# Optimization experiments

Measured on AMD Instinct MI355X. Metric: run time of the kernel, lower is better.

The kernel has to match this reference:

```python
import jax, jax.numpy as jnp
import numpy as np

ALPHA = 0.01        # NoiseLayer gaussian scale
P_FEAT = 0.5        # feature dropout (NoiseLayer and TransForm_W)
P_EDGE = 0.4        # graph_corr edge-value dropout
BN_EPS = 1e-5


def setup_inputs() -> dict:
    key = jax.random.key(0)
    k1, k2, k3, k4 = jax.random.split(key, 4)
    N, E, D_IN, D_H = 100000, 1600000, 512, 128
    data = jax.random.normal(k1, (N, D_IN), dtype=jnp.float32)
    adj_indices = jax.random.randint(k2, (2, E), 0, N, dtype=jnp.int64)
    adj_values = jax.random.uniform(k3, (E,), dtype=jnp.float32)
    W = jax.random.normal(k4, (D_IN, D_H), dtype=jnp.float32) * (6.0 / (D_IN + D_H)) ** 0.5
    gamma = jnp.ones((D_H,), dtype=jnp.float32)
    beta = jnp.zeros((D_H,), dtype=jnp.float32)
    return {"data": data, "adj_indices": adj_indices, "adj_values": adj_values,
            "W": W, "gamma": gamma, "beta": beta}


def reference(data, adj_indices, adj_values, W, gamma, beta):
    N = data.shape[0]
    kn, kd1, kd2, ke = jax.random.split(jax.random.key(42), 4)

    # NoiseLayer: x + alpha*randn, then dropout(p=0.5)
    x = data + ALPHA * jax.random.normal(kn, data.shape, data.dtype)
    keep = 1.0 - P_FEAT
    x = x * jax.random.bernoulli(kd1, keep, x.shape).astype(x.dtype) / keep

    # TransForm_W: dropout(p=0.5) then x @ W  -> [N, hidden]
    x = x * jax.random.bernoulli(kd2, keep, x.shape).astype(x.dtype) / keep
    h = x @ W

    # edge-value dropout (graph_corr=0.4) + sparse spmm via segment_sum
    keep_e = 1.0 - P_EDGE
    vals = adj_values * jax.random.bernoulli(ke, keep_e, adj_values.shape).astype(adj_values.dtype) / keep_e
    row, col = adj_indices[0], adj_indices[1]
    msg = vals[:, None] * h[col]                       # [E, hidden]
    agg = jax.ops.segment_sum(msg, row, num_segments=N)  # [N, hidden]

    # ELU activation
    feat = jax.nn.elu(agg)

    # BatchNorm1d (training mode, batch stats over nodes), view_type='spatial'
    mean = feat.mean(axis=0)
    var = feat.var(axis=0)
    feat = gamma * (feat - mean) * jax.lax.rsqrt(var + BN_EPS) + beta
    return feat
```

## Files before the change

kernel.cpp:

```cpp
#include <hip/hip_runtime.h>
#include <stdint.h>

#define N_NODES 100000
#define D_IN 512
#define D_H 128
#define N_EDGES 1600000

__host__ __device__ __forceinline__ void threefry2x32(uint32_t k0, uint32_t k1,
                                                      uint32_t x0, uint32_t x1,
                                                      uint32_t& o0, uint32_t& o1) {
  uint32_t k2 = k0 ^ k1 ^ 0x1BD11BDAu;
  x0 += k0; x1 += k1;
#if defined(__HIP_DEVICE_COMPILE__)
#define ROTL(v, r) __builtin_rotateleft32((v), (r))
#else
#define ROTL(v, r) (((v) << (r)) | ((v) >> (32 - (r))))
#endif
#define TFR(r) x0 += x1; x1 = ROTL(x1, r); x1 ^= x0;
  TFR(13) TFR(15) TFR(26) TFR(6)
  x0 += k1; x1 += k2 + 1u;
  TFR(17) TFR(29) TFR(16) TFR(24)
  x0 += k2; x1 += k0 + 2u;
  TFR(13) TFR(15) TFR(26) TFR(6)
  x0 += k0; x1 += k1 + 3u;
  TFR(17) TFR(29) TFR(16) TFR(24)
  x0 += k1; x1 += k2 + 4u;
  TFR(13) TFR(15) TFR(26) TFR(6)
  x0 += k2; x1 += k0 + 5u;
#undef TFR
#undef ROTL
  o0 = x0; o1 = x1;
}

__device__ __forceinline__ uint32_t tf_bits(uint32_t k0, uint32_t k1, uint32_t i) {
  uint32_t w0, w1;
  threefry2x32(k0, k1, 0u, i, w0, w1);
  return w0 ^ w1;
}

__device__ __forceinline__ float bits_to_unit(uint32_t b) {
  return __uint_as_float((b >> 9) | 0x3f800000u) - 1.0f;
}

__device__ __forceinline__ unsigned short f2bf(float f) {
  uint32_t b = __float_as_uint(f);
  return (unsigned short)((b + 0x7FFFu + ((b >> 16) & 1u)) >> 16);
}

__device__ __forceinline__ float erfinv_fast(float x) {
  float w = -__logf(fmaf(-x, x, 1.0f));
  float wc = w - 2.5f;
  float p = 2.81022636e-08f;
  p = fmaf(p, wc, 3.43273939e-07f);
  p = fmaf(p, wc, -3.5233877e-06f);
  p = fmaf(p, wc, -4.39150654e-06f);
  p = fmaf(p, wc, 0.00021858087f);
  p = fmaf(p, wc, -0.00125372503f);
  p = fmaf(p, wc, -0.00417768164f);
  p = fmaf(p, wc, 0.246640727f);
  p = fmaf(p, wc, 1.50140941f);
  float wt = fmaf(w, rsqrtf(w), -3.0f);
  float q = -0.000200214257f;
  q = fmaf(q, wt, 0.000100950558f);
  q = fmaf(q, wt, 0.00134934322f);
  q = fmaf(q, wt, -0.00367342844f);
  q = fmaf(q, wt, 0.00573950773f);
  q = fmaf(q, wt, -0.0076224613f);
  q = fmaf(q, wt, 0.00943887047f);
  q = fmaf(q, wt, 1.00167406f);
  q = fmaf(q, wt, 2.83297682f);
  return ((w < 5.0f) ? p : q) * x;
}

#define PE 0.60000002384185791f
#define GS_BLKS 2048

__global__ __launch_bounds__(256) void prep_kernel(
    const int* __restrict__ adj32, int* __restrict__ flag,
    int* __restrict__ counts, float* __restrict__ stats,
    const float* __restrict__ W, unsigned short* __restrict__ Wt) {
  int idx = blockIdx.x * 256 + threadIdx.x;
  if (blockIdx.x == 0 && threadIdx.x < 64) {
    bool hi_zero = (adj32[2 * threadIdx.x + 1] == 0);
    unsigned long long bl = __ballot(hi_zero);
    if (threadIdx.x == 0) *flag = (bl == ~0ull) ? 1 : 0;
  }
  if (idx < N_NODES) counts[idx] = 0;
  if (idx < 256) stats[idx] = 0.0f;
  if (idx < D_IN * D_H) {
    int k = idx >> 7, n = idx & 127;
    Wt[n * 512 + k] = f2bf(W[idx]);
  }
}

#define MAIN_CHUNKS 31250

__global__ __launch_bounds__(256) void fused_kernel(
    const float* __restrict__ data, unsigned short* __restrict__ x,
    const int* __restrict__ adj32, const int* __restrict__ flag,
    int* __restrict__ counts,
    uint32_t kn0, uint32_t kn1, uint32_t kd10, uint32_t kd11,
    uint32_t kd20, uint32_t kd21, uint32_t ke0, uint32_t ke1) {
  __shared__ uint2 queue[4][512];
  __shared__ unsigned short res[4][512];
  const int wave = threadIdx.x >> 6, lane = threadIdx.x & 63;
  for (uint32_t c = blockIdx.x; c < MAIN_CHUNKS; c += gridDim.x) {
    if ((c % 5u) == 4u) {
      uint32_t e = (c / 5u) * 256u + threadIdx.x;
      int fl = *flag;
      int r = fl ? adj32[2 * e] : adj32[e];
      uint32_t eb = tf_bits(ke0, ke1, e);
      if (bits_to_unit(eb) < PE) atomicAdd(&counts[r], 1);
      continue;
    }
    uint32_t gblk = (c / 5u) * 4u + (c % 5u);
    const uint32_t wbase = gblk * 2048u + (uint32_t)wave * 512u;
    const uint32_t i0 = wbase + (uint32_t)lane * 8u;
    float4 d0 = *(const float4*)(data + i0);
    float4 d1 = *(const float4*)(data + i0 + 4);
    float dv[8] = {d0.x, d0.y, d0.z, d0.w, d1.x, d1.y, d1.z, d1.w};
    *(uint4*)(&res[wave][lane * 8]) = make_uint4(0u, 0u, 0u, 0u);

    uint32_t qc = 0;
#pragma unroll
    for (int j = 0; j < 8; ++j) {
      uint32_t ab = tf_bits(kd10, kd11, i0 + (uint32_t)j);
      bool keep = (ab >> 31) == 0u;
      unsigned long long m = __ballot(keep);
      uint32_t below = __builtin_amdgcn_mbcnt_hi(
          (uint32_t)(m >> 32), __builtin_amdgcn_mbcnt_lo((uint32_t)m, 0u));
      if (keep)
        queue[wave][qc + below] =
            make_uint2(__float_as_uint(dv[j]), (uint32_t)(lane * 8 + j));
      qc += (uint32_t)__popcll(m);
    }

    uint32_t qc2 = 0;
    for (uint32_t k0 = 0; k0 < qc; k0 += 64) {
      uint32_t k = k0 + (uint32_t)lane;
      bool act = k < qc;
      uint2 ent = make_uint2(0u, 0u);
      if (act) ent = queue[wave][k];
      uint32_t bb = tf_bits(kd20, kd21, wbase + ent.y);
      bool keep = act && ((bb >> 31) == 0u);
      unsigned long long m = __ballot(keep);
      uint32_t below = __builtin_amdgcn_mbcnt_hi(
          (uint32_t)(m >> 32), __builtin_amdgcn_mbcnt_lo((uint32_t)m, 0u));
      if (keep) queue[wave][qc2 + below] = ent;
      qc2 += (uint32_t)__popcll(m);
    }

    for (uint32_t k0 = 0; k0 < qc2; k0 += 64) {
      uint32_t k = k0 + (uint32_t)lane;
      bool act = k < qc2;
      uint2 ent = make_uint2(0u, 0u);
      if (act) ent = queue[wave][k];
      uint32_t nb = tf_bits(kn0, kn1, wbase + ent.y);
      float f = bits_to_unit(nb);
      float u = fmaf(f, 2.0f, -0.99999994f);
      float z = erfinv_fast(u);
      float val = fmaf(0.0141421356237f, z, __uint_as_float(ent.x));
      unsigned short r = f2bf(val * 4.0f);
      if (act) res[wave][ent.y] = r;
    }

    uint4 rr = *(const uint4*)(&res[wave][lane * 8]);
    *(uint4*)(x + i0) = rr;
  }
}

typedef __attribute__((ext_vector_type(8))) short bf16x8;
typedef __attribute__((ext_vector_type(4))) float f32x4;
typedef _Float16 half8 __attribute__((ext_vector_type(8)));
#define BM 64
#define BK 64
#define LDT 72

__global__ __launch_bounds__(256) void gemm_kernel(
    const unsigned short* __restrict__ x, const unsigned short* __restrict__ Wt,
    unsigned short* __restrict__ hh) {
  __shared__ __align__(16) unsigned short a_lds[BM * LDT];
  __shared__ __align__(16) unsigned short b_lds[128 * LDT];
  const int tid = threadIdx.x;
  const int r0 = blockIdx.x * BM;
  const int wave = tid >> 6, lane = tid & 63;
  const int lane15 = lane & 15, quad = lane >> 4;
  const int waveM = (wave & 1) * 32, waveN = (wave >> 1) * 64;
  f32x4 acc[2][4] = {};
  for (int kc = 0; kc < D_IN; kc += BK) {
    __syncthreads();
    {
      int row = tid >> 2, q = tid & 3;
      int gr = r0 + row;
      uint4 v0 = make_uint4(0, 0, 0, 0), v1 = v0;
      if (gr < N_NODES) {
        const unsigned short* src = x + (size_t)gr * D_IN + kc + q * 16;
        v0 = *(const uint4*)(src);
        v1 = *(const uint4*)(src + 8);
      }
      *(uint4*)(a_lds + row * LDT + q * 16) = v0;
      *(uint4*)(a_lds + row * LDT + q * 16 + 8) = v1;
    }
    {
      int n = tid >> 1, half = tid & 1;
      const uint4* src = (const uint4*)(Wt + n * 512 + kc + half * 32);
      uint4* dst = (uint4*)(b_lds + n * LDT + half * 32);
      dst[0] = src[0]; dst[1] = src[1]; dst[2] = src[2]; dst[3] = src[3];
    }
    __syncthreads();
    for (int ks = 0; ks < BK; ks += 32) {
      bf16x8 afrag[2], bfrag[4];
      for (int m = 0; m < 2; ++m)
        afrag[m] = *(const bf16x8*)(a_lds + (waveM + m * 16 + lane15) * LDT + ks + quad * 8);
      for (int n = 0; n < 4; ++n)
        bfrag[n] = *(const bf16x8*)(b_lds + (waveN + n * 16 + lane15) * LDT + ks + quad * 8);
      for (int m = 0; m < 2; ++m)
        for (int n = 0; n < 4; ++n)
          acc[m][n] = __builtin_amdgcn_mfma_f32_16x16x32_bf16(afrag[m], bfrag[n], acc[m][n], 0, 0, 0);
    }
  }
  for (int m = 0; m < 2; ++m) {
    int growb = r0 + waveM + m * 16 + quad * 4;
    for (int r = 0; r < 4; ++r) {
      int grow = growb + r;
      if (grow < N_NODES)
        for (int n = 0; n < 4; ++n) {
          _Float16 hv = (_Float16)acc[m][n][r];
          hh[(size_t)grow * D_H + waveN + n * 16 + lane15] =
              __builtin_bit_cast(unsigned short, hv);
        }
    }
  }
}

#define SCAN_B 512
#define SCAN_NBLK ((N_NODES + SCAN_B - 1) / SCAN_B)

__global__ __launch_bounds__(256) void scan1_kernel(const int* __restrict__ counts,
                                                    int* __restrict__ rowstart,
                                                    int* __restrict__ bsums) {
  __shared__ int bufA[SCAN_B], bufB[SCAN_B];
  int t = threadIdx.x, b = blockIdx.x;
  int g0 = b * SCAN_B + t, g1 = g0 + 256;
  int v0 = (g0 < N_NODES) ? counts[g0] : 0;
  int v1 = (g1 < N_NODES) ? counts[g1] : 0;
  bufA[t] = v0; bufA[t + 256] = v1;
  __syncthreads();
  int* src = bufA; int* dst = bufB;
  for (int off = 1; off < SCAN_B; off <<= 1) {
    for (int k = t; k < SCAN_B; k += 256)
      dst[k] = src[k] + ((k >= off) ? src[k - off] : 0);
    __syncthreads();
    int* tmp = src; src = dst; dst = tmp;
  }
  if (g0 < N_NODES) rowstart[g0] = src[t] - v0;
  if (g1 < N_NODES) rowstart[g1] = src[t + 256] - v1;
  if (t == 0) bsums[b] = src[SCAN_B - 1];
}

__global__ __launch_bounds__(256) void scan23_kernel(int* __restrict__ rowstart,
                                                     const int* __restrict__ bsums,
                                                     int* __restrict__ cursor) {
  __shared__ int bufA[256], bufB[256];
  __shared__ int bscan_l[256];
  int t = threadIdx.x;
  int v = (t < SCAN_NBLK) ? bsums[t] : 0;
  bufA[t] = v;
  __syncthreads();
  int* src = bufA; int* dst = bufB;
  for (int off = 1; off < 256; off <<= 1) {
    dst[t] = src[t] + ((t >= off) ? src[t - off] : 0);
    __syncthreads();
    int* tmp = src; src = dst; dst = tmp;
  }
  bscan_l[t] = src[t] - v;
  __syncthreads();
  int i = blockIdx.x * 256 + t;
  if (i < N_NODES) {
    int val = rowstart[i] + bscan_l[i / SCAN_B];
    rowstart[i] = val;
    cursor[i] = val;
  }
}

__global__ __launch_bounds__(256) void scatter_kernel(
    const int* __restrict__ adj32, const int* __restrict__ flag,
    const float* __restrict__ vals, int* __restrict__ cursor,
    int* __restrict__ scol, float* __restrict__ sval,
    uint32_t ke0, uint32_t ke1) {
  int fl = *flag;
  uint32_t stride = gridDim.x * 256u;
  for (uint32_t e = blockIdx.x * 256u + threadIdx.x; e < (uint32_t)N_EDGES;
       e += stride) {
    uint32_t eb = tf_bits(ke0, ke1, e);
    if (bits_to_unit(eb) >= PE) continue;
    int r = fl ? adj32[2 * e] : adj32[e];
    int c = fl ? adj32[2 * (N_EDGES + e)] : adj32[N_EDGES + e];
    int pos = atomicAdd(&cursor[r], 1);
    scol[pos] = c;
    sval[pos] = vals[e] / PE;
  }
}

__global__ __launch_bounds__(256) void spmm_stats_kernel(
    const int* __restrict__ scol, const float* __restrict__ sval,
    const int* __restrict__ rowstart, const int* __restrict__ counts,
    const unsigned short* __restrict__ hh, float* __restrict__ agg,
    float* __restrict__ stats) {
  __shared__ float ls[4][128], lq[4][128];
  const int wave = threadIdx.x >> 6, lane = threadIdx.x & 63;
  const int g = lane >> 4, l4 = lane & 15;
  const unsigned short* hp = hh + l4 * 8;
  float es[8] = {}, eq[8] = {};
  const int wstride = gridDim.x * 4;
  for (int r = blockIdx.x * 4 + wave; r < N_NODES; r += wstride) {
    int start = rowstart[r], len = counts[r];
    float acc[8] = {};
    int j = 0;
    for (; j + 8 <= len; j += 8) {
      int e0 = start + j + g, e1 = e0 + 4;
      int c0 = scol[e0], c1 = scol[e1];
      float v0 = sval[e0], v1 = sval[e1];
      uint4 b0 = *(const uint4*)(hp + (size_t)c0 * D_H);
      uint4 b1 = *(const uint4*)(hp + (size_t)c1 * D_H);
      half8 x0 = __builtin_bit_cast(half8, b0);
      half8 x1 = __builtin_bit_cast(half8, b1);
#pragma unroll
      for (int k = 0; k < 8; ++k) {
        acc[k] = fmaf(v0, (float)x0[k], acc[k]);
        acc[k] = fmaf(v1, (float)x1[k], acc[k]);
      }
    }
    if (j + g < len) {
      int e = start + j + g;
      int c = scol[e];
      float v = sval[e];
      uint4 bb = *(const uint4*)(hp + (size_t)c * D_H);
      half8 xv = __builtin_bit_cast(half8, bb);
#pragma unroll
      for (int k = 0; k < 8; ++k) acc[k] = fmaf(v, (float)xv[k], acc[k]);
    }
    if (j + 4 + g < len) {
      int e = start + j + 4 + g;
      int c = scol[e];
      float v = sval[e];
      uint4 bb = *(const uint4*)(hp + (size_t)c * D_H);
      half8 xv = __builtin_bit_cast(half8, bb);
#pragma unroll
      for (int k = 0; k < 8; ++k) acc[k] = fmaf(v, (float)xv[k], acc[k]);
    }
#pragma unroll
    for (int k = 0; k < 8; ++k) {
      acc[k] += __shfl_xor(acc[k], 16, 64);
      acc[k] += __shfl_xor(acc[k], 32, 64);
    }
    if (g == 0) {
      float e8[8];
#pragma unroll
      for (int k = 0; k < 8; ++k) {
        float a = acc[k];
        float e = a > 0.f ? a : expm1f(a);
        e8[k] = e;
        es[k] += e;
        eq[k] += e * e;
      }
      float* op = agg + (size_t)r * D_H + l4 * 8;
      *(float4*)op = make_float4(e8[0], e8[1], e8[2], e8[3]);
      *(float4*)(op + 4) = make_float4(e8[4], e8[5], e8[6], e8[7]);
    }
  }
  if (g == 0) {
#pragma unroll
    for (int k = 0; k < 8; ++k) {
      ls[wave][l4 * 8 + k] = es[k];
      lq[wave][l4 * 8 + k] = eq[k];
    }
  }
  __syncthreads();
  if (threadIdx.x < 128) {
    int t = threadIdx.x;
    float s = ls[0][t] + ls[1][t] + ls[2][t] + ls[3][t];
    float q = lq[0][t] + lq[1][t] + lq[2][t] + lq[3][t];
    atomicAdd(&stats[t], s);
    atomicAdd(&stats[128 + t], q);
  }
}

__global__ __launch_bounds__(256) void bn_kernel(const float* __restrict__ agg,
                                                 const float* __restrict__ stats,
                                                 const float* __restrict__ gamma,
                                                 const float* __restrict__ beta,
                                                 float* __restrict__ out) {
  const float inv_n = 1.0f / (float)N_NODES;
  const int tot4 = N_NODES * D_H / 4;
  int idx0 = blockIdx.x * 256 + threadIdx.x;
  int stride = gridDim.x * 256;
  int f0 = (idx0 * 4) & 127;
  float sc[4], sh[4];
#pragma unroll
  for (int j = 0; j < 4; ++j) {
    int f = f0 + j;
    float mean = stats[f] * inv_n;
    float var = stats[128 + f] * inv_n - mean * mean;
    float gsc = gamma[f] * rsqrtf(var + 1e-5f);
    sc[j] = gsc;
    sh[j] = beta[f] - mean * gsc;
  }
  for (int idx4 = idx0; idx4 < tot4; idx4 += stride) {
    size_t base = (size_t)idx4 * 4;
    float4 a = *(const float4*)(agg + base);
    float4 o;
    o.x = fmaf(a.x, sc[0], sh[0]);
    o.y = fmaf(a.y, sc[1], sh[1]);
    o.z = fmaf(a.z, sc[2], sh[2]);
    o.w = fmaf(a.w, sc[3], sh[3]);
    *(float4*)(out + base) = o;
  }
}

extern "C" void kernel_launch(void* const* d_in, const int* in_sizes, int n_in,
                              void* d_out, int out_size, void* d_ws, size_t ws_size,
                              hipStream_t stream) {
  const float* data = (const float*)d_in[0];
  const int* adj = (const int*)d_in[1];
  const float* vals = (const float*)d_in[2];
  const float* W = (const float*)d_in[3];
  const float* gamma = (const float*)d_in[4];
  const float* beta = (const float*)d_in[5];
  float* out = (float*)d_out;

  char* ws = (char*)d_ws;
  unsigned short* x = (unsigned short*)ws;
  float* agg = (float*)ws;
  int* scol = (int*)(ws + 51200000);
  float* sval = (float*)(ws + 57600000);
  int* rowstart = (int*)(ws + 64000000);
  int* cursor = (int*)(ws + 64400000);
  int* bsums = (int*)(ws + 64800000);
  unsigned short* hh = (unsigned short*)(ws + 102400000);
  unsigned short* Wt = (unsigned short*)(ws + 153600000);
  float* stats = (float*)(ws + 153731072);
  int* flag = (int*)(ws + 153732096);
  int* counts = (int*)(ws + 153733120);

  uint32_t kk[4][2];
  for (uint32_t i = 0; i < 4; ++i) threefry2x32(0u, 42u, 0u, i, kk[i][0], kk[i][1]);
  uint32_t kn0 = kk[0][0], kn1 = kk[0][1];
  uint32_t kd10 = kk[1][0], kd11 = kk[1][1];
  uint32_t kd20 = kk[2][0], kd21 = kk[2][1];
  uint32_t ke0 = kk[3][0], ke1 = kk[3][1];

  prep_kernel<<<391, 256, 0, stream>>>(adj, flag, counts, stats, W, Wt);
  fused_kernel<<<GS_BLKS, 256, 0, stream>>>(
      data, x, adj, flag, counts,
      kn0, kn1, kd10, kd11, kd20, kd21, ke0, ke1);
  gemm_kernel<<<(N_NODES + BM - 1) / BM, 256, 0, stream>>>(x, Wt, hh);
  scan1_kernel<<<SCAN_NBLK, 256, 0, stream>>>(counts, rowstart, bsums);
  scan23_kernel<<<391, 256, 0, stream>>>(rowstart, bsums, cursor);
  scatter_kernel<<<GS_BLKS, 256, 0, stream>>>(adj, flag, vals, cursor, scol, sval, ke0, ke1);
  spmm_stats_kernel<<<GS_BLKS, 256, 0, stream>>>(scol, sval, rowstart, counts, hh, agg, stats);
  bn_kernel<<<GS_BLKS, 256, 0, stream>>>(agg, stats, gamma, beta, out);
}
```

Before: 652.1 us.

## Merge scan, scatter, SpMM and BN into one persistent kernel with grid barriers

```diff
diff --git a/kernel.cpp b/kernel.cpp
--- a/kernel.cpp
+++ b/kernel.cpp
@@ -73,18 +73,19 @@
 }
 
 #define PE 0.60000002384185791f
-#define GS_BLKS 2048
 
 __global__ __launch_bounds__(256) void prep_kernel(
     const int* __restrict__ adj32, int* __restrict__ flag,
     int* __restrict__ counts, float* __restrict__ stats,
-    const float* __restrict__ W, unsigned short* __restrict__ Wt) {
+    const float* __restrict__ W, unsigned short* __restrict__ Wt,
+    int* __restrict__ bar) {
   int idx = blockIdx.x * 256 + threadIdx.x;
   if (blockIdx.x == 0 && threadIdx.x < 64) {
     bool hi_zero = (adj32[2 * threadIdx.x + 1] == 0);
     unsigned long long bl = __ballot(hi_zero);
     if (threadIdx.x == 0) *flag = (bl == ~0ull) ? 1 : 0;
   }
+  if (idx == 0) *bar = 0;
   if (idx < N_NODES) counts[idx] = 0;
   if (idx < 256) stats[idx] = 0.0f;
   if (idx < D_IN * D_H) {
@@ -93,7 +94,9 @@
   }
 }
 
-#define MAIN_CHUNKS 31250
+#define GEN_BLKS 25000
+#define EDGE_BLKS 6250
+#define MAIN_BLKS 31250
 
 __global__ __launch_bounds__(256) void fused_kernel(
     const float* __restrict__ data, unsigned short* __restrict__ x,
@@ -103,70 +106,69 @@
     uint32_t kd20, uint32_t kd21, uint32_t ke0, uint32_t ke1) {
   __shared__ uint2 queue[4][512];
   __shared__ unsigned short res[4][512];
+  int b = blockIdx.x;
+  if ((b % 5) == 4) {
+    uint32_t e = (uint32_t)(b / 5) * 256u + threadIdx.x;
+    int fl = *flag;
+    int r = fl ? adj32[2 * e] : adj32[e];
+    uint32_t eb = tf_bits(ke0, ke1, e);
+    if (bits_to_unit(eb) < PE) atomicAdd(&counts[r], 1);
+    return;
+  }
+  uint32_t gblk = (uint32_t)(b / 5) * 4u + (uint32_t)(b % 5);
   const int wave = threadIdx.x >> 6, lane = threadIdx.x & 63;
-  for (uint32_t c = blockIdx.x; c < MAIN_CHUNKS; c += gridDim.x) {
-    if ((c % 5u) == 4u) {
-      uint32_t e = (c / 5u) * 256u + threadIdx.x;
-      int fl = *flag;
-      int r = fl ? adj32[2 * e] : adj32[e];
-      uint32_t eb = tf_bits(ke0, ke1, e);
-      if (bits_to_unit(eb) < PE) atomicAdd(&counts[r], 1);
-      continue;
-    }
-    uint32_t gblk = (c / 5u) * 4u + (c % 5u);
-    const uint32_t wbase = gblk * 2048u + (uint32_t)wave * 512u;
-    const uint32_t i0 = wbase + (uint32_t)lane * 8u;
-    float4 d0 = *(const float4*)(data + i0);
-    float4 d1 = *(const float4*)(data + i0 + 4);
-    float dv[8] = {d0.x, d0.y, d0.z, d0.w, d1.x, d1.y, d1.z, d1.w};
-    *(uint4*)(&res[wave][lane * 8]) = make_uint4(0u, 0u, 0u, 0u);
-
-    uint32_t qc = 0;
-#pragma unroll
-    for (int j = 0; j < 8; ++j) {
-      uint32_t ab = tf_bits(kd10, kd11, i0 + (uint32_t)j);
-      bool keep = (ab >> 31) == 0u;
-      unsigned long long m = __ballot(keep);
-      uint32_t below = __builtin_amdgcn_mbcnt_hi(
-          (uint32_t)(m >> 32), __builtin_amdgcn_mbcnt_lo((uint32_t)m, 0u));
-      if (keep)
-        queue[wave][qc + below] =
-            make_uint2(__float_as_uint(dv[j]), (uint32_t)(lane * 8 + j));
-      qc += (uint32_t)__popcll(m);
-    }
-
-    uint32_t qc2 = 0;
-    for (uint32_t k0 = 0; k0 < qc; k0 += 64) {
-      uint32_t k = k0 + (uint32_t)lane;
-      bool act = k < qc;
-      uint2 ent = make_uint2(0u, 0u);
-      if (act) ent = queue[wave][k];
-      uint32_t bb = tf_bits(kd20, kd21, wbase + ent.y);
-      bool keep = act && ((bb >> 31) == 0u);
-      unsigned long long m = __ballot(keep);
-      uint32_t below = __builtin_amdgcn_mbcnt_hi(
-          (uint32_t)(m >> 32), __builtin_amdgcn_mbcnt_lo((uint32_t)m, 0u));
-      if (keep) queue[wave][qc2 + below] = ent;
-      qc2 += (uint32_t)__popcll(m);
-    }
-
-    for (uint32_t k0 = 0; k0 < qc2; k0 += 64) {
-      uint32_t k = k0 + (uint32_t)lane;
-      bool act = k < qc2;
-      uint2 ent = make_uint2(0u, 0u);
-      if (act) ent = queue[wave][k];
-      uint32_t nb = tf_bits(kn0, kn1, wbase + ent.y);
-      float f = bits_to_unit(nb);
-      float u = fmaf(f, 2.0f, -0.99999994f);
-      float z = erfinv_fast(u);
-      float val = fmaf(0.0141421356237f, z, __uint_as_float(ent.x));
-      unsigned short r = f2bf(val * 4.0f);
-      if (act) res[wave][ent.y] = r;
-    }
-
-    uint4 rr = *(const uint4*)(&res[wave][lane * 8]);
-    *(uint4*)(x + i0) = rr;
-  }
+  const uint32_t wbase = gblk * 2048u + (uint32_t)wave * 512u;
+  const uint32_t i0 = wbase + (uint32_t)lane * 8u;
+  float4 d0 = *(const float4*)(data + i0);
+  float4 d1 = *(const float4*)(data + i0 + 4);
+  float dv[8] = {d0.x, d0.y, d0.z, d0.w, d1.x, d1.y, d1.z, d1.w};
+  *(uint4*)(&res[wave][lane * 8]) = make_uint4(0u, 0u, 0u, 0u);
+
+  uint32_t qc = 0;
+#pragma unroll
+  for (int j = 0; j < 8; ++j) {
+    uint32_t ab = tf_bits(kd10, kd11, i0 + (uint32_t)j);
+    bool keep = (ab >> 31) == 0u;
+    unsigned long long m = __ballot(keep);
+    uint32_t below = __builtin_amdgcn_mbcnt_hi(
+        (uint32_t)(m >> 32), __builtin_amdgcn_mbcnt_lo((uint32_t)m, 0u));
+    if (keep)
+      queue[wave][qc + below] =
+          make_uint2(__float_as_uint(dv[j]), (uint32_t)(lane * 8 + j));
+    qc += (uint32_t)__popcll(m);
+  }
+
+  uint32_t qc2 = 0;
+  for (uint32_t k0 = 0; k0 < qc; k0 += 64) {
+    uint32_t k = k0 + (uint32_t)lane;
+    bool act = k < qc;
+    uint2 ent = make_uint2(0u, 0u);
+    if (act) ent = queue[wave][k];
+    uint32_t bb = tf_bits(kd20, kd21, wbase + ent.y);
+    bool keep = act && ((bb >> 31) == 0u);
+    unsigned long long m = __ballot(keep);
+    uint32_t below = __builtin_amdgcn_mbcnt_hi(
+        (uint32_t)(m >> 32), __builtin_amdgcn_mbcnt_lo((uint32_t)m, 0u));
+    if (keep) queue[wave][qc2 + below] = ent;
+    qc2 += (uint32_t)__popcll(m);
+  }
+
+  for (uint32_t k0 = 0; k0 < qc2; k0 += 64) {
+    uint32_t k = k0 + (uint32_t)lane;
+    bool act = k < qc2;
+    uint2 ent = make_uint2(0u, 0u);
+    if (act) ent = queue[wave][k];
+    uint32_t nb = tf_bits(kn0, kn1, wbase + ent.y);
+    float f = bits_to_unit(nb);
+    float u = fmaf(f, 2.0f, -0.99999994f);
+    float z = erfinv_fast(u);
+    float val = fmaf(0.0141421356237f, z, __uint_as_float(ent.x));
+    unsigned short r = f2bf(val * 4.0f);
+    if (act) res[wave][ent.y] = r;
+  }
+
+  uint4 rr = *(const uint4*)(&res[wave][lane * 8]);
+  *(uint4*)(x + i0) = rr;
 }
 
 typedef __attribute__((ext_vector_type(8))) short bf16x8;
@@ -235,186 +237,196 @@
 
 #define SCAN_B 512
 #define SCAN_NBLK ((N_NODES + SCAN_B - 1) / SCAN_B)
-
-__global__ __launch_bounds__(256) void scan1_kernel(const int* __restrict__ counts,
-                                                    int* __restrict__ rowstart,
-                                                    int* __restrict__ bsums) {
+#define POST_BLKS 1024
+
+__device__ __forceinline__ void grid_barrier(int* bar, int target) {
+  __syncthreads();
+  if (threadIdx.x == 0) {
+    __threadfence();
+    __hip_atomic_fetch_add(bar, 1, __ATOMIC_ACQ_REL, __HIP_MEMORY_SCOPE_AGENT);
+    while (__hip_atomic_load(bar, __ATOMIC_ACQUIRE, __HIP_MEMORY_SCOPE_AGENT) <
+           target)
+      __builtin_amdgcn_s_sleep(2);
+  }
+  __syncthreads();
+}
+
+__global__ __launch_bounds__(256, 4) void post_kernel(
+    int* __restrict__ counts, int* __restrict__ rowstart,
+    int* __restrict__ bsums, int* __restrict__ cursor,
+    const int* __restrict__ adj32, const int* __restrict__ flag,
+    const float* __restrict__ vals, int* __restrict__ scol,
+    float* __restrict__ sval, const unsigned short* __restrict__ hh,
+    float* __restrict__ agg, float* __restrict__ stats,
+    const float* __restrict__ gamma, const float* __restrict__ beta,
+    float* __restrict__ out, int* __restrict__ bar,
+    uint32_t ke0, uint32_t ke1) {
   __shared__ int bufA[SCAN_B], bufB[SCAN_B];
-  int t = threadIdx.x, b = blockIdx.x;
-  int g0 = b * SCAN_B + t, g1 = g0 + 256;
-  int v0 = (g0 < N_NODES) ? counts[g0] : 0;
-  int v1 = (g1 < N_NODES) ? counts[g1] : 0;
-  bufA[t] = v0; bufA[t + 256] = v1;
-  __syncthreads();
-  int* src = bufA; int* dst = bufB;
-  for (int off = 1; off < SCAN_B; off <<= 1) {
-    for (int k = t; k < SCAN_B; k += 256)
-      dst[k] = src[k] + ((k >= off) ? src[k - off] : 0);
-    __syncthreads();
-    int* tmp = src; src = dst; dst = tmp;
-  }
-  if (g0 < N_NODES) rowstart[g0] = src[t] - v0;
-  if (g1 < N_NODES) rowstart[g1] = src[t + 256] - v1;
-  if (t == 0) bsums[b] = src[SCAN_B - 1];
-}
-
-__global__ __launch_bounds__(256) void scan23_kernel(int* __restrict__ rowstart,
-                                                     const int* __restrict__ bsums,
-                                                     int* __restrict__ cursor) {
-  __shared__ int bufA[256], bufB[256];
   __shared__ int bscan_l[256];
-  int t = threadIdx.x;
-  int v = (t < SCAN_NBLK) ? bsums[t] : 0;
-  bufA[t] = v;
-  __syncthreads();
-  int* src = bufA; int* dst = bufB;
-  for (int off = 1; off < 256; off <<= 1) {
-    dst[t] = src[t] + ((t >= off) ? src[t - off] : 0);
-    __syncthreads();
-    int* tmp = src; src = dst; dst = tmp;
-  }
-  bscan_l[t] = src[t] - v;
-  __syncthreads();
-  int i = blockIdx.x * 256 + t;
-  if (i < N_NODES) {
-    int val = rowstart[i] + bscan_l[i / SCAN_B];
-    rowstart[i] = val;
-    cursor[i] = val;
-  }
-}
-
-__global__ __launch_bounds__(256) void scatter_kernel(
-    const int* __restrict__ adj32, const int* __restrict__ flag,
-    const float* __restrict__ vals, int* __restrict__ cursor,
-    int* __restrict__ scol, float* __restrict__ sval,
-    uint32_t ke0, uint32_t ke1) {
-  int fl = *flag;
-  uint32_t stride = gridDim.x * 256u;
-  for (uint32_t e = blockIdx.x * 256u + threadIdx.x; e < (uint32_t)N_EDGES;
-       e += stride) {
-    uint32_t eb = tf_bits(ke0, ke1, e);
-    if (bits_to_unit(eb) >= PE) continue;
-    int r = fl ? adj32[2 * e] : adj32[e];
-    int c = fl ? adj32[2 * (N_EDGES + e)] : adj32[N_EDGES + e];
-    int pos = atomicAdd(&cursor[r], 1);
-    scol[pos] = c;
-    sval[pos] = vals[e] / PE;
-  }
-}
-
-__global__ __launch_bounds__(256) void spmm_stats_kernel(
-    const int* __restrict__ scol, const float* __restrict__ sval,
-    const int* __restrict__ rowstart, const int* __restrict__ counts,
-    const unsigned short* __restrict__ hh, float* __restrict__ agg,
-    float* __restrict__ stats) {
   __shared__ float ls[4][128], lq[4][128];
-  const int wave = threadIdx.x >> 6, lane = threadIdx.x & 63;
-  const int g = lane >> 4, l4 = lane & 15;
-  const unsigned short* hp = hh + l4 * 8;
-  float es[8] = {}, eq[8] = {};
-  const int wstride = gridDim.x * 4;
-  for (int r = blockIdx.x * 4 + wave; r < N_NODES; r += wstride) {
-    int start = rowstart[r], len = counts[r];
-    float acc[8] = {};
-    int j = 0;
-    for (; j + 8 <= len; j += 8) {
-      int e0 = start + j + g, e1 = e0 + 4;
-      int c0 = scol[e0], c1 = scol[e1];
-      float v0 = sval[e0], v1 = sval[e1];
-      uint4 b0 = *(const uint4*)(hp + (size_t)c0 * D_H);
-      uint4 b1 = *(const uint4*)(hp + (size_t)c1 * D_H);
-      half8 x0 = __builtin_bit_cast(half8, b0);
-      half8 x1 = __builtin_bit_cast(half8, b1);
+  const int t = threadIdx.x;
+
+  for (int sb = blockIdx.x; sb < SCAN_NBLK; sb += gridDim.x) {
+    int g0 = sb * SCAN_B + t, g1 = g0 + 256;
+    int v0 = (g0 < N_NODES) ? counts[g0] : 0;
+    int v1 = (g1 < N_NODES) ? counts[g1] : 0;
+    bufA[t] = v0; bufA[t + 256] = v1;
+    __syncthreads();
+    int* src = bufA; int* dst = bufB;
+    for (int off = 1; off < SCAN_B; off <<= 1) {
+      for (int k = t; k < SCAN_B; k += 256)
+        dst[k] = src[k] + ((k >= off) ? src[k - off] : 0);
+      __syncthreads();
+      int* tmp = src; src = dst; dst = tmp;
+    }
+    if (g0 < N_NODES) rowstart[g0] = src[t] - v0;
+    if (g1 < N_NODES) rowstart[g1] = src[t + 256] - v1;
+    if (t == 0) bsums[sb] = src[SCAN_B - 1];
+    __syncthreads();
+  }
+  grid_barrier(bar, gridDim.x * 1);
+
+  {
+    int v = (t < SCAN_NBLK) ? bsums[t] : 0;
+    bufA[t] = v;
+    __syncthreads();
+    int* src = bufA; int* dst = bufB;
+    for (int off = 1; off < 256; off <<= 1) {
+      dst[t] = src[t] + ((t >= off) ? src[t - off] : 0);
+      __syncthreads();
+      int* tmp = src; src = dst; dst = tmp;
+    }
+    bscan_l[t] = src[t] - v;
+    __syncthreads();
+    for (int i = blockIdx.x * 256 + t; i < N_NODES; i += gridDim.x * 256) {
+      int val = rowstart[i] + bscan_l[i / SCAN_B];
+      rowstart[i] = val;
+      cursor[i] = val;
+    }
+  }
+  grid_barrier(bar, gridDim.x * 2);
+
+  {
+    int fl = *flag;
+    uint32_t stride = gridDim.x * 256u;
+    for (uint32_t e = blockIdx.x * 256u + t; e < (uint32_t)N_EDGES; e += stride) {
+      uint32_t eb = tf_bits(ke0, ke1, e);
+      if (bits_to_unit(eb) >= PE) continue;
+      int r = fl ? adj32[2 * e] : adj32[e];
+      int c = fl ? adj32[2 * (N_EDGES + e)] : adj32[N_EDGES + e];
+      int pos = atomicAdd(&cursor[r], 1);
+      scol[pos] = c;
+      sval[pos] = vals[e] / PE;
+    }
+  }
+  grid_barrier(bar, gridDim.x * 3);
+
+  {
+    const int wave = t >> 6, lane = t & 63;
+    const int g = lane >> 4, l4 = lane & 15;
+    const unsigned short* hp = hh + l4 * 8;
+    float es[8] = {}, eq[8] = {};
+    const int wstride = gridDim.x * 4;
+    for (int r = blockIdx.x * 4 + wave; r < N_NODES; r += wstride) {
+      int start = rowstart[r], len = counts[r];
+      float acc[8] = {};
+      int j = 0;
+      for (; j + 8 <= len; j += 8) {
+        int e0 = start + j + g, e1 = e0 + 4;
+        int c0 = scol[e0], c1 = scol[e1];
+        float v0 = sval[e0], v1 = sval[e1];
+        uint4 b0 = *(const uint4*)(hp + (size_t)c0 * D_H);
+        uint4 b1 = *(const uint4*)(hp + (size_t)c1 * D_H);
+        half8 x0 = __builtin_bit_cast(half8, b0);
+        half8 x1 = __builtin_bit_cast(half8, b1);
+#pragma unroll
+        for (int k = 0; k < 8; ++k) {
+          acc[k] = fmaf(v0, (float)x0[k], acc[k]);
+          acc[k] = fmaf(v1, (float)x1[k], acc[k]);
+        }
+      }
+      if (j + g < len) {
+        int e = start + j + g;
+        int c = scol[e];
+        float v = sval[e];
+        uint4 bb = *(const uint4*)(hp + (size_t)c * D_H);
+        half8 xv = __builtin_bit_cast(half8, bb);
+#pragma unroll
+        for (int k = 0; k < 8; ++k) acc[k] = fmaf(v, (float)xv[k], acc[k]);
+      }
+      if (j + 4 + g < len) {
+        int e = start + j + 4 + g;
+        int c = scol[e];
+        float v = sval[e];
+        uint4 bb = *(const uint4*)(hp + (size_t)c * D_H);
+        half8 xv = __builtin_bit_cast(half8, bb);
+#pragma unroll
+        for (int k = 0; k < 8; ++k) acc[k] = fmaf(v, (float)xv[k], acc[k]);
+      }
 #pragma unroll
       for (int k = 0; k < 8; ++k) {
-        acc[k] = fmaf(v0, (float)x0[k], acc[k]);
-        acc[k] = fmaf(v1, (float)x1[k], acc[k]);
-      }
-    }
-    if (j + g < len) {
-      int e = start + j + g;
-      int c = scol[e];
-      float v = sval[e];
-      uint4 bb = *(const uint4*)(hp + (size_t)c * D_H);
-      half8 xv = __builtin_bit_cast(half8, bb);
-#pragma unroll
-      for (int k = 0; k < 8; ++k) acc[k] = fmaf(v, (float)xv[k], acc[k]);
-    }
-    if (j + 4 + g < len) {
-      int e = start + j + 4 + g;
-      int c = scol[e];
-      float v = sval[e];
-      uint4 bb = *(const uint4*)(hp + (size_t)c * D_H);
-      half8 xv = __builtin_bit_cast(half8, bb);
-#pragma unroll
-      for (int k = 0; k < 8; ++k) acc[k] = fmaf(v, (float)xv[k], acc[k]);
-    }
-#pragma unroll
-    for (int k = 0; k < 8; ++k) {
-      acc[k] += __shfl_xor(acc[k], 16, 64);
-      acc[k] += __shfl_xor(acc[k], 32, 64);
-    }
+        acc[k] += __shfl_xor(acc[k], 16, 64);
+        acc[k] += __shfl_xor(acc[k], 32, 64);
+      }
+      if (g == 0) {
+        float e8[8];
+#pragma unroll
+        for (int k = 0; k < 8; ++k) {
+          float a = acc[k];
+          float e = a > 0.f ? a : expm1f(a);
+          e8[k] = e;
+          es[k] += e;
+          eq[k] += e * e;
+        }
+        float* op = agg + (size_t)r * D_H + l4 * 8;
+        *(float4*)op = make_float4(e8[0], e8[1], e8[2], e8[3]);
+        *(float4*)(op + 4) = make_float4(e8[4], e8[5], e8[6], e8[7]);
+      }
+    }
+    __syncthreads();
     if (g == 0) {
-      float e8[8];
 #pragma unroll
       for (int k = 0; k < 8; ++k) {
-        float a = acc[k];
-        float e = a > 0.f ? a : expm1f(a);
-        e8[k] = e;
-        es[k] += e;
-        eq[k] += e * e;
-      }
-      float* op = agg + (size_t)r * D_H + l4 * 8;
-      *(float4*)op = make_float4(e8[0], e8[1], e8[2], e8[3]);
-      *(float4*)(op + 4) = make_float4(e8[4], e8[5], e8[6], e8[7]);
-    }
-  }
-  if (g == 0) {
-#pragma unroll
-    for (int k = 0; k < 8; ++k) {
-      ls[wave][l4 * 8 + k] = es[k];
-      lq[wave][l4 * 8 + k] = eq[k];
-    }
-  }
-  __syncthreads();
-  if (threadIdx.x < 128) {
-    int t = threadIdx.x;
-    float s = ls[0][t] + ls[1][t] + ls[2][t] + ls[3][t];
-    float q = lq[0][t] + lq[1][t] + lq[2][t] + lq[3][t];
-    atomicAdd(&stats[t], s);
-    atomicAdd(&stats[128 + t], q);
-  }
-}
-
-__global__ __launch_bounds__(256) void bn_kernel(const float* __restrict__ agg,
-                                                 const float* __restrict__ stats,
-                                                 const float* __restrict__ gamma,
-                                                 const float* __restrict__ beta,
-                                                 float* __restrict__ out) {
-  const float inv_n = 1.0f / (float)N_NODES;
-  const int tot4 = N_NODES * D_H / 4;
-  int idx0 = blockIdx.x * 256 + threadIdx.x;
-  int stride = gridDim.x * 256;
-  int f0 = (idx0 * 4) & 127;
-  float sc[4], sh[4];
-#pragma unroll
-  for (int j = 0; j < 4; ++j) {
-    int f = f0 + j;
-    float mean = stats[f] * inv_n;
-    float var = stats[128 + f] * inv_n - mean * mean;
-    float gsc = gamma[f] * rsqrtf(var + 1e-5f);
-    sc[j] = gsc;
-    sh[j] = beta[f] - mean * gsc;
-  }
-  for (int idx4 = idx0; idx4 < tot4; idx4 += stride) {
-    size_t base = (size_t)idx4 * 4;
-    float4 a = *(const float4*)(agg + base);
-    float4 o;
-    o.x = fmaf(a.x, sc[0], sh[0]);
-    o.y = fmaf(a.y, sc[1], sh[1]);
-    o.z = fmaf(a.z, sc[2], sh[2]);
-    o.w = fmaf(a.w, sc[3], sh[3]);
-    *(float4*)(out + base) = o;
+        ls[wave][l4 * 8 + k] = es[k];
+        lq[wave][l4 * 8 + k] = eq[k];
+      }
+    }
+    __syncthreads();
+    if (t < 128) {
+      float s = ls[0][t] + ls[1][t] + ls[2][t] + ls[3][t];
+      float q = lq[0][t] + lq[1][t] + lq[2][t] + lq[3][t];
+      atomicAdd(&stats[t], s);
+      atomicAdd(&stats[128 + t], q);
+    }
+  }
+  grid_barrier(bar, gridDim.x * 4);
+
+  {
+    const float inv_n = 1.0f / (float)N_NODES;
+    const int tot4 = N_NODES * D_H / 4;
+    int idx0 = blockIdx.x * 256 + t;
+    int stride = gridDim.x * 256;
+    int f0 = (idx0 * 4) & 127;
+    float sc[4], sh[4];
+#pragma unroll
+    for (int j = 0; j < 4; ++j) {
+      int f = f0 + j;
+      float mean = stats[f] * inv_n;
+      float var = stats[128 + f] * inv_n - mean * mean;
+      float gsc = gamma[f] * rsqrtf(var + 1e-5f);
+      sc[j] = gsc;
+      sh[j] = beta[f] - mean * gsc;
+    }
+    for (int idx4 = idx0; idx4 < tot4; idx4 += stride) {
+      size_t base = (size_t)idx4 * 4;
+      float4 a = *(const float4*)(agg + base);
+      float4 o;
+      o.x = fmaf(a.x, sc[0], sh[0]);
+      o.y = fmaf(a.y, sc[1], sh[1]);
+      o.z = fmaf(a.z, sc[2], sh[2]);
+      o.w = fmaf(a.w, sc[3], sh[3]);
+      *(float4*)(out + base) = o;
+    }
   }
 }
 
@@ -441,6 +453,7 @@
   unsigned short* Wt = (unsigned short*)(ws + 153600000);
   float* stats = (float*)(ws + 153731072);
   int* flag = (int*)(ws + 153732096);
+  int* bar = (int*)(ws + 153732100);
   int* counts = (int*)(ws + 153733120);
 
   uint32_t kk[4][2];
@@ -450,14 +463,12 @@
   uint32_t kd20 = kk[2][0], kd21 = kk[2][1];
   uint32_t ke0 = kk[3][0], ke1 = kk[3][1];
 
-  prep_kernel<<<391, 256, 0, stream>>>(adj, flag, counts, stats, W, Wt);
-  fused_kernel<<<GS_BLKS, 256, 0, stream>>>(
+  prep_kernel<<<391, 256, 0, stream>>>(adj, flag, counts, stats, W, Wt, bar);
+  fused_kernel<<<MAIN_BLKS, 256, 0, stream>>>(
       data, x, adj, flag, counts,
       kn0, kn1, kd10, kd11, kd20, kd21, ke0, ke1);
   gemm_kernel<<<(N_NODES + BM - 1) / BM, 256, 0, stream>>>(x, Wt, hh);
-  scan1_kernel<<<SCAN_NBLK, 256, 0, stream>>>(counts, rowstart, bsums);
-  scan23_kernel<<<391, 256, 0, stream>>>(rowstart, bsums, cursor);
-  scatter_kernel<<<GS_BLKS, 256, 0, stream>>>(adj, flag, vals, cursor, scol, sval, ke0, ke1);
-  spmm_stats_kernel<<<GS_BLKS, 256, 0, stream>>>(scol, sval, rowstart, counts, hh, agg, stats);
-  bn_kernel<<<GS_BLKS, 256, 0, stream>>>(agg, stats, gamma, beta, out);
-}
+  post_kernel<<<POST_BLKS, 256, 0, stream>>>(
+      counts, rowstart, bsums, cursor, adj, flag, vals, scol, sval, hh,
+      agg, stats, gamma, beta, out, bar, ke0, ke1);
+}
```

Result: slower. 1.080 ms (+65.6%).

## Launch one block per work item and map one row per 16-lane group in SpMM

Applied to the files above, without the earlier changes.

```diff
diff --git a/kernel.cpp b/kernel.cpp
--- a/kernel.cpp
+++ b/kernel.cpp
@@ -73,7 +73,6 @@
 }
 
 #define PE 0.60000002384185791f
-#define GS_BLKS 2048
 
 __global__ __launch_bounds__(256) void prep_kernel(
     const int* __restrict__ adj32, int* __restrict__ flag,
@@ -93,7 +92,7 @@
   }
 }
 
-#define MAIN_CHUNKS 31250
+#define MAIN_BLKS 31250
 
 __global__ __launch_bounds__(256) void fused_kernel(
     const float* __restrict__ data, unsigned short* __restrict__ x,
@@ -103,70 +102,69 @@
     uint32_t kd20, uint32_t kd21, uint32_t ke0, uint32_t ke1) {
   __shared__ uint2 queue[4][512];
   __shared__ unsigned short res[4][512];
+  int b = blockIdx.x;
+  if ((b % 5) == 4) {
+    uint32_t e = (uint32_t)(b / 5) * 256u + threadIdx.x;
+    int fl = *flag;
+    int r = fl ? adj32[2 * e] : adj32[e];
+    uint32_t eb = tf_bits(ke0, ke1, e);
+    if (bits_to_unit(eb) < PE) atomicAdd(&counts[r], 1);
+    return;
+  }
+  uint32_t gblk = (uint32_t)(b / 5) * 4u + (uint32_t)(b % 5);
   const int wave = threadIdx.x >> 6, lane = threadIdx.x & 63;
-  for (uint32_t c = blockIdx.x; c < MAIN_CHUNKS; c += gridDim.x) {
-    if ((c % 5u) == 4u) {
-      uint32_t e = (c / 5u) * 256u + threadIdx.x;
-      int fl = *flag;
-      int r = fl ? adj32[2 * e] : adj32[e];
-      uint32_t eb = tf_bits(ke0, ke1, e);
-      if (bits_to_unit(eb) < PE) atomicAdd(&counts[r], 1);
-      continue;
-    }
-    uint32_t gblk = (c / 5u) * 4u + (c % 5u);
-    const uint32_t wbase = gblk * 2048u + (uint32_t)wave * 512u;
-    const uint32_t i0 = wbase + (uint32_t)lane * 8u;
-    float4 d0 = *(const float4*)(data + i0);
-    float4 d1 = *(const float4*)(data + i0 + 4);
-    float dv[8] = {d0.x, d0.y, d0.z, d0.w, d1.x, d1.y, d1.z, d1.w};
-    *(uint4*)(&res[wave][lane * 8]) = make_uint4(0u, 0u, 0u, 0u);
-
-    uint32_t qc = 0;
-#pragma unroll
-    for (int j = 0; j < 8; ++j) {
-      uint32_t ab = tf_bits(kd10, kd11, i0 + (uint32_t)j);
-      bool keep = (ab >> 31) == 0u;
-      unsigned long long m = __ballot(keep);
-      uint32_t below = __builtin_amdgcn_mbcnt_hi(
-          (uint32_t)(m >> 32), __builtin_amdgcn_mbcnt_lo((uint32_t)m, 0u));
-      if (keep)
-        queue[wave][qc + below] =
-            make_uint2(__float_as_uint(dv[j]), (uint32_t)(lane * 8 + j));
-      qc += (uint32_t)__popcll(m);
-    }
-
-    uint32_t qc2 = 0;
-    for (uint32_t k0 = 0; k0 < qc; k0 += 64) {
-      uint32_t k = k0 + (uint32_t)lane;
-      bool act = k < qc;
-      uint2 ent = make_uint2(0u, 0u);
-      if (act) ent = queue[wave][k];
-      uint32_t bb = tf_bits(kd20, kd21, wbase + ent.y);
-      bool keep = act && ((bb >> 31) == 0u);
-      unsigned long long m = __ballot(keep);
-      uint32_t below = __builtin_amdgcn_mbcnt_hi(
-          (uint32_t)(m >> 32), __builtin_amdgcn_mbcnt_lo((uint32_t)m, 0u));
-      if (keep) queue[wave][qc2 + below] = ent;
-      qc2 += (uint32_t)__popcll(m);
-    }
-
-    for (uint32_t k0 = 0; k0 < qc2; k0 += 64) {
-      uint32_t k = k0 + (uint32_t)lane;
-      bool act = k < qc2;
-      uint2 ent = make_uint2(0u, 0u);
-      if (act) ent = queue[wave][k];
-      uint32_t nb = tf_bits(kn0, kn1, wbase + ent.y);
-      float f = bits_to_unit(nb);
-      float u = fmaf(f, 2.0f, -0.99999994f);
-      float z = erfinv_fast(u);
-      float val = fmaf(0.0141421356237f, z, __uint_as_float(ent.x));
-      unsigned short r = f2bf(val * 4.0f);
-      if (act) res[wave][ent.y] = r;
-    }
-
-    uint4 rr = *(const uint4*)(&res[wave][lane * 8]);
-    *(uint4*)(x + i0) = rr;
-  }
+  const uint32_t wbase = gblk * 2048u + (uint32_t)wave * 512u;
+  const uint32_t i0 = wbase + (uint32_t)lane * 8u;
+  float4 d0 = *(const float4*)(data + i0);
+  float4 d1 = *(const float4*)(data + i0 + 4);
+  float dv[8] = {d0.x, d0.y, d0.z, d0.w, d1.x, d1.y, d1.z, d1.w};
+  *(uint4*)(&res[wave][lane * 8]) = make_uint4(0u, 0u, 0u, 0u);
+
+  uint32_t qc = 0;
+#pragma unroll
+  for (int j = 0; j < 8; ++j) {
+    uint32_t ab = tf_bits(kd10, kd11, i0 + (uint32_t)j);
+    bool keep = (ab >> 31) == 0u;
+    unsigned long long m = __ballot(keep);
+    uint32_t below = __builtin_amdgcn_mbcnt_hi(
+        (uint32_t)(m >> 32), __builtin_amdgcn_mbcnt_lo((uint32_t)m, 0u));
+    if (keep)
+      queue[wave][qc + below] =
+          make_uint2(__float_as_uint(dv[j]), (uint32_t)(lane * 8 + j));
+    qc += (uint32_t)__popcll(m);
+  }
+
+  uint32_t qc2 = 0;
+  for (uint32_t k0 = 0; k0 < qc; k0 += 64) {
+    uint32_t k = k0 + (uint32_t)lane;
+    bool act = k < qc;
+    uint2 ent = make_uint2(0u, 0u);
+    if (act) ent = queue[wave][k];
+    uint32_t bb = tf_bits(kd20, kd21, wbase + ent.y);
+    bool keep = act && ((bb >> 31) == 0u);
+    unsigned long long m = __ballot(keep);
+    uint32_t below = __builtin_amdgcn_mbcnt_hi(
+        (uint32_t)(m >> 32), __builtin_amdgcn_mbcnt_lo((uint32_t)m, 0u));
+    if (keep) queue[wave][qc2 + below] = ent;
+    qc2 += (uint32_t)__popcll(m);
+  }
+
+  for (uint32_t k0 = 0; k0 < qc2; k0 += 64) {
+    uint32_t k = k0 + (uint32_t)lane;
+    bool act = k < qc2;
+    uint2 ent = make_uint2(0u, 0u);
+    if (act) ent = queue[wave][k];
+    uint32_t nb = tf_bits(kn0, kn1, wbase + ent.y);
+    float f = bits_to_unit(nb);
+    float u = fmaf(f, 2.0f, -0.99999994f);
+    float z = erfinv_fast(u);
+    float val = fmaf(0.0141421356237f, z, __uint_as_float(ent.x));
+    unsigned short r = f2bf(val * 4.0f);
+    if (act) res[wave][ent.y] = r;
+  }
+
+  uint4 rr = *(const uint4*)(&res[wave][lane * 8]);
+  *(uint4*)(x + i0) = rr;
 }
 
 typedef __attribute__((ext_vector_type(8))) short bf16x8;
@@ -288,18 +286,16 @@
     const float* __restrict__ vals, int* __restrict__ cursor,
     int* __restrict__ scol, float* __restrict__ sval,
     uint32_t ke0, uint32_t ke1) {
+  uint32_t e = blockIdx.x * 256u + threadIdx.x;
+  if (e >= (uint32_t)N_EDGES) return;
+  uint32_t eb = tf_bits(ke0, ke1, e);
+  if (bits_to_unit(eb) >= PE) return;
   int fl = *flag;
-  uint32_t stride = gridDim.x * 256u;
-  for (uint32_t e = blockIdx.x * 256u + threadIdx.x; e < (uint32_t)N_EDGES;
-       e += stride) {
-    uint32_t eb = tf_bits(ke0, ke1, e);
-    if (bits_to_unit(eb) >= PE) continue;
-    int r = fl ? adj32[2 * e] : adj32[e];
-    int c = fl ? adj32[2 * (N_EDGES + e)] : adj32[N_EDGES + e];
-    int pos = atomicAdd(&cursor[r], 1);
-    scol[pos] = c;
-    sval[pos] = vals[e] / PE;
-  }
+  int r = fl ? adj32[2 * e] : adj32[e];
+  int c = fl ? adj32[2 * (N_EDGES + e)] : adj32[N_EDGES + e];
+  int pos = atomicAdd(&cursor[r], 1);
+  scol[pos] = c;
+  sval[pos] = vals[e] / PE;
 }
 
 __global__ __launch_bounds__(256) void spmm_stats_kernel(
@@ -308,66 +304,54 @@
     const unsigned short* __restrict__ hh, float* __restrict__ agg,
     float* __restrict__ stats) {
   __shared__ float ls[4][128], lq[4][128];
-  const int wave = threadIdx.x >> 6, lane = threadIdx.x & 63;
+  const int t = threadIdx.x;
+  const int wave = t >> 6, lane = t & 63;
   const int g = lane >> 4, l4 = lane & 15;
   const unsigned short* hp = hh + l4 * 8;
+  const int r = blockIdx.x * 16 + wave * 4 + g;
   float es[8] = {}, eq[8] = {};
-  const int wstride = gridDim.x * 4;
-  for (int r = blockIdx.x * 4 + wave; r < N_NODES; r += wstride) {
+  {
     int start = rowstart[r], len = counts[r];
     float acc[8] = {};
-    int j = 0;
-    for (; j + 8 <= len; j += 8) {
-      int e0 = start + j + g, e1 = e0 + 4;
-      int c0 = scol[e0], c1 = scol[e1];
-      float v0 = sval[e0], v1 = sval[e1];
-      uint4 b0 = *(const uint4*)(hp + (size_t)c0 * D_H);
-      uint4 b1 = *(const uint4*)(hp + (size_t)c1 * D_H);
-      half8 x0 = __builtin_bit_cast(half8, b0);
-      half8 x1 = __builtin_bit_cast(half8, b1);
-#pragma unroll
-      for (int k = 0; k < 8; ++k) {
-        acc[k] = fmaf(v0, (float)x0[k], acc[k]);
-        acc[k] = fmaf(v1, (float)x1[k], acc[k]);
+    for (int j = 0; j < len; j += 4) {
+      int cc[4]; float vv[4];
+#pragma unroll
+      for (int u = 0; u < 4; ++u) {
+        int jj = j + u;
+        int e = start + (jj < len ? jj : len - 1);
+        cc[u] = scol[e];
+        vv[u] = (jj < len) ? sval[e] : 0.0f;
       }
-    }
-    if (j + g < len) {
-      int e = start + j + g;
-      int c = scol[e];
-      float v = sval[e];
-      uint4 bb = *(const uint4*)(hp + (size_t)c * D_H);
-      half8 xv = __builtin_bit_cast(half8, bb);
-#pragma unroll
-      for (int k = 0; k < 8; ++k) acc[k] = fmaf(v, (float)xv[k], acc[k]);
-    }
-    if (j + 4 + g < len) {
-      int e = start + j + 4 + g;
-      int c = scol[e];
-      float v = sval[e];
-      uint4 bb = *(const uint4*)(hp + (size_t)c * D_H);
-      half8 xv = __builtin_bit_cast(half8, bb);
-#pragma unroll
-      for (int k = 0; k < 8; ++k) acc[k] = fmaf(v, (float)xv[k], acc[k]);
-    }
+      uint4 bb[4];
+#pragma unroll
+      for (int u = 0; u < 4; ++u)
+        bb[u] = *(const uint4*)(hp + (size_t)cc[u] * D_H);
+#pragma unroll
+      for (int u = 0; u < 4; ++u) {
+        half8 xv = __builtin_bit_cast(half8, bb[u]);
+#pragma unroll
+        for (int k = 0; k < 8; ++k) acc[k] = fmaf(vv[u], (float)xv[k], acc[k]);
+      }
+    }
+    float e8[8];
 #pragma unroll
     for (int k = 0; k < 8; ++k) {
-      acc[k] += __shfl_xor(acc[k], 16, 64);
-      acc[k] += __shfl_xor(acc[k], 32, 64);
-    }
-    if (g == 0) {
-      float e8[8];
-#pragma unroll
-      for (int k = 0; k < 8; ++k) {
-        float a = acc[k];
-        float e = a > 0.f ? a : expm1f(a);
-        e8[k] = e;
-        es[k] += e;
-        eq[k] += e * e;
-      }
-      float* op = agg + (size_t)r * D_H + l4 * 8;
-      *(float4*)op = make_float4(e8[0], e8[1], e8[2], e8[3]);
-      *(float4*)(op + 4) = make_float4(e8[4], e8[5], e8[6], e8[7]);
-    }
+      float a = acc[k];
+      float e = a > 0.f ? a : expm1f(a);
+      e8[k] = e;
+      es[k] += e;
+      eq[k] += e * e;
+    }
+    float* op = agg + (size_t)r * D_H + l4 * 8;
+    *(float4*)op = make_float4(e8[0], e8[1], e8[2], e8[3]);
+    *(float4*)(op + 4) = make_float4(e8[4], e8[5], e8[6], e8[7]);
+  }
+#pragma unroll
+  for (int k = 0; k < 8; ++k) {
+    es[k] += __shfl_xor(es[k], 16, 64);
+    es[k] += __shfl_xor(es[k], 32, 64);
+    eq[k] += __shfl_xor(eq[k], 16, 64);
+    eq[k] += __shfl_xor(eq[k], 32, 64);
   }
   if (g == 0) {
 #pragma unroll
@@ -377,8 +361,7 @@
     }
   }
   __syncthreads();
-  if (threadIdx.x < 128) {
-    int t = threadIdx.x;
+  if (t < 128) {
     float s = ls[0][t] + ls[1][t] + ls[2][t] + ls[3][t];
     float q = lq[0][t] + lq[1][t] + lq[2][t] + lq[3][t];
     atomicAdd(&stats[t], s);
@@ -451,13 +434,13 @@
   uint32_t ke0 = kk[3][0], ke1 = kk[3][1];
 
   prep_kernel<<<391, 256, 0, stream>>>(adj, flag, counts, stats, W, Wt);
-  fused_kernel<<<GS_BLKS, 256, 0, stream>>>(
+  fused_kernel<<<MAIN_BLKS, 256, 0, stream>>>(
       data, x, adj, flag, counts,
       kn0, kn1, kd10, kd11, kd20, kd21, ke0, ke1);
   gemm_kernel<<<(N_NODES + BM - 1) / BM, 256, 0, stream>>>(x, Wt, hh);
   scan1_kernel<<<SCAN_NBLK, 256, 0, stream>>>(counts, rowstart, bsums);
   scan23_kernel<<<391, 256, 0, stream>>>(rowstart, bsums, cursor);
-  scatter_kernel<<<GS_BLKS, 256, 0, stream>>>(adj, flag, vals, cursor, scol, sval, ke0, ke1);
-  spmm_stats_kernel<<<GS_BLKS, 256, 0, stream>>>(scol, sval, rowstart, counts, hh, agg, stats);
-  bn_kernel<<<GS_BLKS, 256, 0, stream>>>(agg, stats, gamma, beta, out);
-}
+  scatter_kernel<<<6250, 256, 0, stream>>>(adj, flag, vals, cursor, scol, sval, ke0, ke1);
+  spmm_stats_kernel<<<6250, 256, 0, stream>>>(scol, sval, rowstart, counts, hh, agg, stats);
+  bn_kernel<<<2048, 256, 0, stream>>>(agg, stats, gamma, beta, out);
+}
```

After: 700.0 us. 7.4% more time.
